# Kernel tuning notes

Hardware: AMD Instinct MI355X
Metric: run time of the kernel (lower is better)

The kernel has to match this reference:

```python
import jax, jax.numpy as jnp
import numpy as np

V, B, T, C, H, L = 32000, 4, 1024, 1024, 16, 8
HS = C // H  # head_size = 64


def _ln(x, g, b):
    m = x.mean(-1, keepdims=True)
    v = x.var(-1, keepdims=True)
    return (x - m) / jnp.sqrt(v + 1e-5) * g + b


def setup_inputs() -> dict:
    key = jax.random.key(0)
    ks = jax.random.split(key, 24)
    s = 0.02
    inp = {
        "idx": jax.random.randint(ks[0], (B, T), 0, V, dtype=jnp.int64),
        "tok_emb": jax.random.normal(ks[1], (V, C), jnp.float32) * s,
        "pos_emb": jax.random.normal(ks[2], (T, C), jnp.float32) * s,
        "Wq": jax.random.normal(ks[3], (L, H, C, HS), jnp.float32) * s,
        "Wk": jax.random.normal(ks[4], (L, H, C, HS), jnp.float32) * s,
        "Wv": jax.random.normal(ks[5], (L, H, C, HS), jnp.float32) * s,
        "Ph_w": jax.random.normal(ks[6], (L, H, HS, C), jnp.float32) * s,
        "Ph_b": jnp.zeros((L, H, C), jnp.float32),
        "Pm_w": jax.random.normal(ks[7], (L, C, C), jnp.float32) * s,
        "Pm_b": jnp.zeros((L, C), jnp.float32),
        "ln1_g": jnp.ones((L, C), jnp.float32),
        "ln1_b": jnp.zeros((L, C), jnp.float32),
        "ln2_g": jnp.ones((L, C), jnp.float32),
        "ln2_b": jnp.zeros((L, C), jnp.float32),
        "W1": jax.random.normal(ks[8], (L, C, 4 * C), jnp.float32) * s,
        "b1": jnp.zeros((L, 4 * C), jnp.float32),
        "W2": jax.random.normal(ks[9], (L, 4 * C, C), jnp.float32) * s,
        "b2": jnp.zeros((L, C), jnp.float32),
        "lnf_g": jnp.ones((C,), jnp.float32),
        "lnf_b": jnp.zeros((C,), jnp.float32),
        "head_w": jax.random.normal(ks[10], (C, V), jnp.float32) * s,
        "head_b": jnp.zeros((V,), jnp.float32),
    }
    return inp


def reference(idx, tok_emb, pos_emb, Wq, Wk, Wv, Ph_w, Ph_b, Pm_w, Pm_b,
              ln1_g, ln1_b, ln2_g, ln2_b, W1, b1, W2, b2, lnf_g, lnf_b,
              head_w, head_b):
    Bx, Tx = idx.shape
    x = tok_emb[idx] + pos_emb[:Tx]  # [B,T,C]
    mask = jnp.tril(jnp.ones((Tx, Tx), bool))
    scale = x.shape[-1] ** -0.5  # NOTE: original scales by n_embd**-0.5, not head_size
    n_layers = Wq.shape[0]
    for l in range(n_layers):
        xn = _ln(x, ln1_g[l], ln1_b[l])
        q = jnp.einsum('btc,hcs->bhts', xn, Wq[l])
        k = jnp.einsum('btc,hcs->bhts', xn, Wk[l])
        v = jnp.einsum('btc,hcs->bhts', xn, Wv[l])
        wei = jnp.einsum('bhts,bhus->bhtu', q, k) * scale
        wei = jnp.where(mask, wei, -jnp.inf)
        wei = jax.nn.softmax(wei, axis=-1)
        o = jnp.einsum('bhtu,bhus->bhts', wei, v)  # [B,H,T,HS]
        per = jnp.einsum('bhts,hsc->bhtc', o, Ph_w[l]) + Ph_b[l][None, :, None, :]
        sa = per.sum(axis=1) @ Pm_w[l] + Pm_b[l]  # combine heads, final proj
        x = x + sa
        xn2 = _ln(x, ln2_g[l], ln2_b[l])
        h = jax.nn.gelu(xn2 @ W1[l] + b1[l], approximate=False)
        x = x + h @ W2[l] + b2[l]
    x = _ln(x, lnf_g, lnf_b)
    return x @ head_w + head_b  # logits [B,T,V]
```

## Files before the change

kernel.cpp:

```cpp
#include <hip/hip_runtime.h>
#include <hip/hip_bf16.h>
#include <math.h>

static constexpr int V = 32000, B = 4, T = 1024, C = 1024, H = 16, NL = 8, HS = 64;
static constexpr int M = B * T;

typedef __bf16 bf16x8 __attribute__((ext_vector_type(8)));
typedef __bf16 bf16x4 __attribute__((ext_vector_type(4)));
typedef float f32x4 __attribute__((ext_vector_type(4)));

#define AS1 __attribute__((address_space(1)))
#define AS3 __attribute__((address_space(3)))

__global__ void k_embed(const int* __restrict__ idx, const float* __restrict__ tok,
                        const float* __restrict__ pos, float* __restrict__ x) {
  int g = blockIdx.x * blockDim.x + threadIdx.x;
  if (g >= M * C / 4) return;
  int c4 = g & 255;
  int bt = g >> 8;
  int t = bt & (T - 1);
  int row = idx[bt];
  float4 tv = *(const float4*)(tok + (size_t)row * C + c4 * 4);
  float4 pv = *(const float4*)(pos + (size_t)t * C + c4 * 4);
  float4 o;
  o.x = tv.x + pv.x; o.y = tv.y + pv.y; o.z = tv.z + pv.z; o.w = tv.w + pv.w;
  *(float4*)(x + (size_t)bt * C + c4 * 4) = o;
}

__global__ __launch_bounds__(256) void k_ln_bf(const float* __restrict__ x, const float* __restrict__ g,
                                               const float* __restrict__ b, __hip_bfloat16* __restrict__ y) {
  int row = blockIdx.x, tid = threadIdx.x;
  float4 v = ((const float4*)(x + (size_t)row * C))[tid];
  float s = v.x + v.y + v.z + v.w;
  float ss = v.x * v.x + v.y * v.y + v.z * v.z + v.w * v.w;
  for (int off = 32; off > 0; off >>= 1) {
    s += __shfl_down(s, off);
    ss += __shfl_down(ss, off);
  }
  __shared__ float sb[4], qb[4];
  int wid = tid >> 6;
  if ((tid & 63) == 0) { sb[wid] = s; qb[wid] = ss; }
  __syncthreads();
  float st = sb[0] + sb[1] + sb[2] + sb[3];
  float qt = qb[0] + qb[1] + qb[2] + qb[3];
  float mean = st * (1.0f / C);
  float var = qt * (1.0f / C) - mean * mean;
  float rstd = rsqrtf(var + 1e-5f);
  float4 gv = ((const float4*)g)[tid];
  float4 bv = ((const float4*)b)[tid];
  union { __hip_bfloat16 h[4]; ushort4 u; } pk;
  pk.h[0] = __float2bfloat16((v.x - mean) * rstd * gv.x + bv.x);
  pk.h[1] = __float2bfloat16((v.y - mean) * rstd * gv.y + bv.y);
  pk.h[2] = __float2bfloat16((v.z - mean) * rstd * gv.z + bv.z);
  pk.h[3] = __float2bfloat16((v.w - mean) * rstd * gv.w + bv.w);
  *(ushort4*)(y + (size_t)row * C + tid * 4) = pk.u;
}

__device__ __forceinline__ void transp_block(const float* __restrict__ in, __hip_bfloat16* __restrict__ out,
                                             int K, int N, int bx, int by, float (*t)[65]) {
  int n0 = bx * 64, k0 = by * 64;
  int tx = threadIdx.x & 15, ty = threadIdx.x >> 4;
#pragma unroll
  for (int i = 0; i < 64; i += 16) {
    float4 v = *(const float4*)(in + (size_t)(k0 + ty + i) * N + n0 + tx * 4);
    t[ty + i][tx * 4 + 0] = v.x;
    t[ty + i][tx * 4 + 1] = v.y;
    t[ty + i][tx * 4 + 2] = v.z;
    t[ty + i][tx * 4 + 3] = v.w;
  }
  __syncthreads();
#pragma unroll
  for (int i = 0; i < 64; i += 16) {
    int n = ty + i;
    union { __hip_bfloat16 h[4]; ushort4 u; } pk;
#pragma unroll
    for (int j = 0; j < 4; ++j) pk.h[j] = __float2bfloat16(t[tx * 4 + j][n]);
    *(ushort4*)(out + (size_t)(n0 + n) * K + k0 + tx * 4) = pk.u;
  }
}

__global__ __launch_bounds__(256) void k_transp(const float* __restrict__ in, __hip_bfloat16* __restrict__ out,
                                                int K, int N) {
  __shared__ float t[64][65];
  transp_block(in, out, K, N, blockIdx.x, blockIdx.y, t);
}

__global__ __launch_bounds__(256) void k_prep(const float* __restrict__ Wq, const float* __restrict__ Wk,
                                              const float* __restrict__ Wv, const float* __restrict__ Pm,
                                              const float* __restrict__ Ph, const float* __restrict__ W1,
                                              const float* __restrict__ W2,
                                              __hip_bfloat16* __restrict__ qkvw, __hip_bfloat16* __restrict__ pmT,
                                              __hip_bfloat16* __restrict__ phB, __hip_bfloat16* __restrict__ w1T,
                                              __hip_bfloat16* __restrict__ w2T) {
  __shared__ float tls[64][65];
  int bid = blockIdx.x;
  if (bid < 768) {
    int bx = bid & 15, z = bid >> 4;
    int sel = z >> 4, h = z & 15;
    const float* W = sel == 0 ? Wq : (sel == 1 ? Wk : Wv);
    const float* in = W + (size_t)h * C * HS;
    __hip_bfloat16* o = qkvw + ((size_t)sel * 1024 + h * 64) * C;
    int k0 = bx * 64;
    int tx = threadIdx.x & 15, ty = threadIdx.x >> 4;
#pragma unroll
    for (int i = 0; i < 64; i += 16) {
      float4 v = *(const float4*)(in + (size_t)(k0 + ty + i) * HS + tx * 4);
      tls[ty + i][tx * 4 + 0] = v.x;
      tls[ty + i][tx * 4 + 1] = v.y;
      tls[ty + i][tx * 4 + 2] = v.z;
      tls[ty + i][tx * 4 + 3] = v.w;
    }
    __syncthreads();
#pragma unroll
    for (int i = 0; i < 64; i += 16) {
      int n = ty + i;
      union { __hip_bfloat16 h4[4]; ushort4 u; } pk;
#pragma unroll
      for (int j = 0; j < 4; ++j) pk.h4[j] = __float2bfloat16(tls[tx * 4 + j][n]);
      *(ushort4*)(o + (size_t)n * C + k0 + tx * 4) = pk.u;
    }
  } else if (bid < 1024) {
    int r = bid - 768;
    transp_block(Pm, pmT, C, C, r & 15, r >> 4, tls);
  } else if (bid < 2048) {
    int g = (bid - 1024) * 256 + threadIdx.x;
    float4 v = ((const float4*)Ph)[g];
    union { __hip_bfloat16 h[4]; ushort4 u; } pk;
    pk.h[0] = __float2bfloat16(v.x);
    pk.h[1] = __float2bfloat16(v.y);
    pk.h[2] = __float2bfloat16(v.z);
    pk.h[3] = __float2bfloat16(v.w);
    ((ushort4*)phB)[g] = pk.u;
  } else if (bid < 3072) {
    int r = bid - 2048;
    transp_block(W1, w1T, C, 4 * C, r & 63, r >> 6, tls);
  } else {
    int r = bid - 3072;
    transp_block(W2, w2T, 4 * C, C, r & 15, r >> 4, tls);
  }
}

__global__ __launch_bounds__(256) void k_biasc(const float* __restrict__ phb, const float* __restrict__ Pm,
                                               const float* __restrict__ Pmb, float* __restrict__ bc) {
  __shared__ float bs[1024];
  __shared__ float red[4][64];
  int tid = threadIdx.x;
#pragma unroll
  for (int q = 0; q < 4; ++q) {
    int c = tid * 4 + q;
    float s = 0.0f;
    for (int h = 0; h < H; ++h) s += phb[(size_t)h * C + c];
    bs[c] = s;
  }
  __syncthreads();
  int c = blockIdx.x * 64 + (tid & 63);
  int part = tid >> 6;
  float s = 0.0f;
  for (int j = part * 256; j < part * 256 + 256; ++j) s += bs[j] * Pm[(size_t)j * C + c];
  red[part][tid & 63] = s;
  __syncthreads();
  if (tid < 64)
    bc[blockIdx.x * 64 + tid] = Pmb[blockIdx.x * 64 + tid] + red[0][tid] + red[1][tid] + red[2][tid] + red[3][tid];
}

template <int BIAS, int GELU, int RES, int OUTBF>
__global__ __launch_bounds__(256) void k_gemm_bf(const __hip_bfloat16* __restrict__ A,
                                                 const __hip_bfloat16* __restrict__ Bt,
                                                 void* Cout, const float* __restrict__ bias,
                                                 const float* res, int N, int K) {
  __shared__ __align__(16) __hip_bfloat16 As[128 * 32];
  __shared__ __align__(16) __hip_bfloat16 Bs[128 * 32];
  int bm = blockIdx.y * 128, bn = blockIdx.x * 128;
  int tid = threadIdx.x;
  int w = tid >> 6, l = tid & 63;
  int wr = (w >> 1) * 64, wc = (w & 1) * 64;
  int lr = l >> 2;
  int lk = (l & 3) * 8;
  int fr = l & 15;
  int fk = (l >> 4) * 8;
  const __hip_bfloat16* Ag = A + (size_t)bm * K;
  const __hip_bfloat16* Bg = Bt + (size_t)bn * K;
  f32x4 acc[4][4];
#pragma unroll
  for (int m = 0; m < 4; ++m)
#pragma unroll
    for (int n = 0; n < 4; ++n) acc[m][n] = (f32x4){0.f, 0.f, 0.f, 0.f};

  for (int k0 = 0; k0 < K; k0 += 32) {
    __syncthreads();
#pragma unroll
    for (int i = 0; i < 2; ++i) {
      int seg = w * 2 + i;
      int r = seg * 16 + lr;
      __builtin_amdgcn_global_load_lds((const AS1 void*)(Ag + (size_t)r * K + k0 + lk),
                                       (AS3 void*)(As + seg * 512), 16, 0, 0);
      __builtin_amdgcn_global_load_lds((const AS1 void*)(Bg + (size_t)r * K + k0 + lk),
                                       (AS3 void*)(Bs + seg * 512), 16, 0, 0);
    }
    __syncthreads();
    bf16x8 af[4], bfr[4];
#pragma unroll
    for (int m = 0; m < 4; ++m) af[m] = *(const bf16x8*)(As + ((size_t)(wr + m * 16 + fr)) * 32 + fk);
#pragma unroll
    for (int n = 0; n < 4; ++n) bfr[n] = *(const bf16x8*)(Bs + ((size_t)(wc + n * 16 + fr)) * 32 + fk);
#pragma unroll
    for (int m = 0; m < 4; ++m)
#pragma unroll
      for (int n = 0; n < 4; ++n)
        acc[m][n] = __builtin_amdgcn_mfma_f32_16x16x32_bf16(af[m], bfr[n], acc[m][n], 0, 0, 0);
  }
  int crow0 = (l >> 4) * 4;
  int ccol = l & 15;
#pragma unroll
  for (int m = 0; m < 4; ++m) {
    int row = bm + wr + m * 16 + crow0;
#pragma unroll
    for (int n = 0; n < 4; ++n) {
      int col = bn + wc + n * 16 + ccol;
      float bv = BIAS ? bias[col] : 0.0f;
#pragma unroll
      for (int r = 0; r < 4; ++r) {
        float v = acc[m][n][r] + bv;
        if (GELU) v = 0.5f * v * (1.0f + erff(v * 0.70710678118f));
        if (RES) v += res[(size_t)(row + r) * N + col];
        if (OUTBF)
          ((__hip_bfloat16*)Cout)[(size_t)(row + r) * N + col] = __float2bfloat16(v);
        else
          ((float*)Cout)[(size_t)(row + r) * N + col] = v;
      }
    }
  }
}

template <int BIAS, int GELU, int RES, int OUTBF>
__global__ __launch_bounds__(512, 2) void k_gemm256(const __hip_bfloat16* __restrict__ Ah,
                                                    const __hip_bfloat16* __restrict__ Bth,
                                                    void* Cout, const float* __restrict__ bias,
                                                    const float* res, int N, int K) {
  __shared__ __align__(16) __bf16 As[2][2 * 8192];
  __shared__ __align__(16) __bf16 Bs[2][2 * 8192];
  const __bf16* A = (const __bf16*)Ah;
  const __bf16* Bt = (const __bf16*)Bth;
  const int nx = N >> 8;
  const int bid = blockIdx.x;
  const int sw = ((bid & 7) * ((int)gridDim.x >> 3)) + (bid >> 3);
  const int bn = (sw % nx) << 8;
  const int bm = (sw / nx) << 8;
  const int tid = threadIdx.x, w = tid >> 6, l = tid & 63;
  const int wm = w >> 2, wn = w & 3;
  const int fr = l & 15, fg = l >> 4;
  const int srow = w * 32 + (l >> 2);
  const int scole = ((((l & 3) << 4) ^ ((l & 8) << 2) ^ (l & 16)) >> 1);
  const __bf16* Ag = A + (size_t)(bm + srow) * K + scole;
  const __bf16* Bg = Bt + (size_t)(bn + srow) * K + scole;
  const int arow = wm * 128 + fr;
  const int brow = wn * 64 + fr;
  const int kswz = ((fr & 2) << 4) | ((fr & 4) << 2);

  f32x4 acc[8][4];
#pragma unroll
  for (int m = 0; m < 8; ++m)
#pragma unroll
    for (int n = 0; n < 4; ++n) acc[m][n] = (f32x4){0.f, 0.f, 0.f, 0.f};

  auto stage = [&](int bufi, int half, int t) {
    size_t kb = (size_t)t * 64 + half * 32;
#pragma unroll
    for (int jj = 0; jj < 2; ++jj) {
      __builtin_amdgcn_global_load_lds((const AS1 void*)(Ag + (size_t)jj * 16 * K + kb),
                                       (AS3 void*)(&As[bufi][half * 8192 + (w * 32 + jj * 16) * 32]), 16, 0, 0);
      __builtin_amdgcn_global_load_lds((const AS1 void*)(Bg + (size_t)jj * 16 * K + kb),
                                       (AS3 void*)(&Bs[bufi][half * 8192 + (w * 32 + jj * 16) * 32]), 16, 0, 0);
    }
  };

#define RD_A(MG, HALF) \
  (*(const bf16x8*)(&As[cb][(HALF) * 8192 + (arow + (MG) * 16) * 32 + (((fg * 16) ^ kswz) >> 1)]))
#define RD_B(NG, HALF) \
  (*(const bf16x8*)(&Bs[cb][(HALF) * 8192 + (brow + (NG) * 16) * 32 + (((fg * 16) ^ kswz) >> 1)]))

  const int NT = K >> 6;
  stage(0, 0, 0);
  stage(0, 1, 0);

  for (int t = 0; t < NT; ++t) {
    const int cb = t & 1;
    const int nb = cb ^ 1;
    bf16x8 af[8], bv[4];

    asm volatile("s_waitcnt vmcnt(4)" ::: "memory");
    __builtin_amdgcn_s_barrier();
    __builtin_amdgcn_sched_barrier(0);
#pragma unroll
    for (int m = 0; m < 8; ++m) af[m] = RD_A(m, 0);
#pragma unroll
    for (int n = 0; n < 4; ++n) bv[n] = RD_B(n, 0);
    if (t + 1 < NT) stage(nb, 0, t + 1);
    __builtin_amdgcn_s_setprio(1);
#pragma unroll
    for (int m = 0; m < 8; ++m)
#pragma unroll
      for (int n = 0; n < 4; ++n)
        acc[m][n] = __builtin_amdgcn_mfma_f32_16x16x32_bf16(af[m], bv[n], acc[m][n], 0, 0, 0);
    __builtin_amdgcn_s_setprio(0);

    if (t + 1 < NT)
      asm volatile("s_waitcnt vmcnt(4)" ::: "memory");
    else
      asm volatile("s_waitcnt vmcnt(0)" ::: "memory");
    __builtin_amdgcn_s_barrier();
    __builtin_amdgcn_sched_barrier(0);
#pragma unroll
    for (int m = 0; m < 8; ++m) af[m] = RD_A(m, 1);
#pragma unroll
    for (int n = 0; n < 4; ++n) bv[n] = RD_B(n, 1);
    if (t + 1 < NT) stage(nb, 1, t + 1);
    __builtin_amdgcn_s_setprio(1);
#pragma unroll
    for (int m = 0; m < 8; ++m)
#pragma unroll
      for (int n = 0; n < 4; ++n)
        acc[m][n] = __builtin_amdgcn_mfma_f32_16x16x32_bf16(af[m], bv[n], acc[m][n], 0, 0, 0);
    __builtin_amdgcn_s_setprio(0);
  }
#undef RD_A
#undef RD_B

#pragma unroll
  for (int mg = 0; mg < 8; ++mg) {
    int row = bm + wm * 128 + mg * 16 + fg * 4;
#pragma unroll
    for (int n = 0; n < 4; ++n) {
      int col = bn + wn * 64 + n * 16 + fr;
      float bvx = BIAS ? bias[col] : 0.0f;
#pragma unroll
      for (int r = 0; r < 4; ++r) {
        float v = acc[mg][n][r] + bvx;
        if (GELU) v = 0.5f * v * (1.0f + erff(v * 0.70710678118f));
        if (RES) v += res[(size_t)(row + r) * N + col];
        if (OUTBF)
          ((__hip_bfloat16*)Cout)[(size_t)(row + r) * N + col] = __float2bfloat16(v);
        else
          ((float*)Cout)[(size_t)(row + r) * N + col] = v;
      }
    }
  }
}

__global__ __launch_bounds__(256) void k_attn(const __hip_bfloat16* __restrict__ qkvh,
                                              __hip_bfloat16* __restrict__ o) {
  const __bf16* qkv = (const __bf16*)qkvh;
  int qi = blockIdx.x;
  int bh = blockIdx.y;
  int b = bh >> 4, h = bh & 15;
  int tid = threadIdx.x;
  int w = tid >> 6, l = tid & 63;
  int fr = l & 15, fg = l >> 4;
  int qw = qi * 64 + w * 16;

  __shared__ __align__(16) __bf16 Ks[32][72];
  __shared__ __align__(16) __bf16 Vs[32][76];
  __shared__ __align__(16) __bf16 Ps[4][16][40];

  const size_t bT = (size_t)b * T;
  bf16x8 a_q[2];
  {
    const __bf16* qp = qkv + (bT + qw + fr) * 3072 + h * 64 + fg * 8;
    a_q[0] = *(const bf16x8*)qp;
    a_q[1] = *(const bf16x8*)(qp + 32);
  }
  f32x4 acc_o[4];
#pragma unroll
  for (int n = 0; n < 4; ++n) acc_o[n] = (f32x4){0.f, 0.f, 0.f, 0.f};
  float mrow[4] = {-1e30f, -1e30f, -1e30f, -1e30f};
  float lrow[4] = {0.f, 0.f, 0.f, 0.f};

  int sr = tid >> 3;
  int sc = (tid & 7) * 8;
  int ntile = (qi + 1) * 2;
  for (int t = 0; t < ntile; ++t) {
    int kv0 = t * 32;
    __syncthreads();
    {
      const __bf16* kp = qkv + (bT + kv0 + sr) * 3072 + 1024 + h * 64 + sc;
      bf16x8 k8 = *(const bf16x8*)kp;
      bf16x8 v8 = *(const bf16x8*)(kp + 1024);
      *(bf16x8*)&Ks[sr][sc] = k8;
      *(bf16x4*)&Vs[sr][sc] = __builtin_shufflevector(v8, v8, 0, 1, 2, 3);
      *(bf16x4*)&Vs[sr][sc + 4] = __builtin_shufflevector(v8, v8, 4, 5, 6, 7);
    }
    __syncthreads();
    if (kv0 > qw + 15) continue;

    f32x4 s0 = (f32x4){0.f, 0.f, 0.f, 0.f}, s1 = s0;
    s0 = __builtin_amdgcn_mfma_f32_16x16x32_bf16(a_q[0], *(const bf16x8*)&Ks[fr][fg * 8], s0, 0, 0, 0);
    s0 = __builtin_amdgcn_mfma_f32_16x16x32_bf16(a_q[1], *(const bf16x8*)&Ks[fr][32 + fg * 8], s0, 0, 0, 0);
    s1 = __builtin_amdgcn_mfma_f32_16x16x32_bf16(a_q[0], *(const bf16x8*)&Ks[16 + fr][fg * 8], s1, 0, 0, 0);
    s1 = __builtin_amdgcn_mfma_f32_16x16x32_bf16(a_q[1], *(const bf16x8*)&Ks[16 + fr][32 + fg * 8], s1, 0, 0, 0);

    int qrow = qw + fg * 4;
#pragma unroll
    for (int r = 0; r < 4; ++r) { s0[r] *= 0.03125f; s1[r] *= 0.03125f; }
    if (kv0 + 31 > qw) {
#pragma unroll
      for (int r = 0; r < 4; ++r) {
        if (kv0 + fr > qrow + r) s0[r] = -1e30f;
        if (kv0 + 16 + fr > qrow + r) s1[r] = -1e30f;
      }
    }
    float tm[4], psum[4], alpha[4];
#pragma unroll
    for (int r = 0; r < 4; ++r) tm[r] = fmaxf(s0[r], s1[r]);
#pragma unroll
    for (int off = 1; off < 16; off <<= 1)
#pragma unroll
      for (int r = 0; r < 4; ++r) tm[r] = fmaxf(tm[r], __shfl_xor(tm[r], off));
#pragma unroll
    for (int r = 0; r < 4; ++r) {
      float mnew = fmaxf(mrow[r], tm[r]);
      alpha[r] = __expf(mrow[r] - mnew);
      mrow[r] = mnew;
      float p0 = __expf(s0[r] - mnew);
      float p1 = __expf(s1[r] - mnew);
      s0[r] = p0; s1[r] = p1;
      psum[r] = p0 + p1;
    }
#pragma unroll
    for (int off = 1; off < 16; off <<= 1)
#pragma unroll
      for (int r = 0; r < 4; ++r) psum[r] += __shfl_xor(psum[r], off);
#pragma unroll
    for (int r = 0; r < 4; ++r) lrow[r] = lrow[r] * alpha[r] + psum[r];
#pragma unroll
    for (int n = 0; n < 4; ++n)
#pragma unroll
      for (int r = 0; r < 4; ++r) acc_o[n][r] *= alpha[r];

#pragma unroll
    for (int r = 0; r < 4; ++r) {
      Ps[w][fg * 4 + r][fr] = (__bf16)s0[r];
      Ps[w][fg * 4 + r][16 + fr] = (__bf16)s1[r];
    }
    bf16x8 a_p = *(const bf16x8*)&Ps[w][fr][fg * 8];
#pragma unroll
    for (int n = 0; n < 4; ++n) {
      bf16x8 bvv;
#pragma unroll
      for (int j = 0; j < 8; ++j) bvv[j] = Vs[fg * 8 + j][n * 16 + fr];
      acc_o[n] = __builtin_amdgcn_mfma_f32_16x16x32_bf16(a_p, bvv, acc_o[n], 0, 0, 0);
    }
  }
  float inv[4];
#pragma unroll
  for (int r = 0; r < 4; ++r) inv[r] = 1.0f / lrow[r];
  __bf16* ob = (__bf16*)o;
#pragma unroll
  for (int n = 0; n < 4; ++n)
#pragma unroll
    for (int r = 0; r < 4; ++r)
      ob[(bT + qw + fg * 4 + r) * 1024 + h * 64 + n * 16 + fr] = (__bf16)(acc_o[n][r] * inv[r]);
}

extern "C" void kernel_launch(void* const* d_in, const int* in_sizes, int n_in,
                              void* d_out, int out_size, void* d_ws, size_t ws_size,
                              hipStream_t stream) {
  const int* idx = (const int*)d_in[0];
  const float* tok = (const float*)d_in[1];
  const float* pos = (const float*)d_in[2];
  const float* Wq = (const float*)d_in[3];
  const float* Wk = (const float*)d_in[4];
  const float* Wv = (const float*)d_in[5];
  const float* Phw = (const float*)d_in[6];
  const float* Phb = (const float*)d_in[7];
  const float* Pmw = (const float*)d_in[8];
  const float* Pmb = (const float*)d_in[9];
  const float* ln1g = (const float*)d_in[10];
  const float* ln1b = (const float*)d_in[11];
  const float* ln2g = (const float*)d_in[12];
  const float* ln2b = (const float*)d_in[13];
  const float* W1 = (const float*)d_in[14];
  const float* b1 = (const float*)d_in[15];
  const float* W2 = (const float*)d_in[16];
  const float* b2 = (const float*)d_in[17];
  const float* lnfg = (const float*)d_in[18];
  const float* lnfb = (const float*)d_in[19];
  const float* headw = (const float*)d_in[20];
  const float* headb = (const float*)d_in[21];
  float* out = (float*)d_out;

  char* p = (char*)d_ws;
  float* x = (float*)p;                        p += (size_t)M * C * 4;
  float* bcv = (float*)p;                      p += 4096;
  char* layer_region = p;
  __hip_bfloat16* qkvb = (__hip_bfloat16*)p;   p += (size_t)M * 3072 * 2;
  __hip_bfloat16* ob = (__hip_bfloat16*)p;     p += (size_t)M * C * 2;
  __hip_bfloat16* hb = (__hip_bfloat16*)p;     p += (size_t)M * 4 * C * 2;
  __hip_bfloat16* xn = (__hip_bfloat16*)p;     p += (size_t)M * C * 2;
  __hip_bfloat16* qkvw = (__hip_bfloat16*)p;   p += (size_t)3 * C * C * 2;
  __hip_bfloat16* pmT = (__hip_bfloat16*)p;    p += (size_t)C * C * 2;
  __hip_bfloat16* phB = (__hip_bfloat16*)p;    p += (size_t)C * C * 2;
  __hip_bfloat16* wcombT = (__hip_bfloat16*)p; p += (size_t)C * C * 2;
  __hip_bfloat16* w1T = (__hip_bfloat16*)p;    p += (size_t)4 * C * C * 2;
  __hip_bfloat16* w2T = (__hip_bfloat16*)p;    p += (size_t)4 * C * C * 2;
  __hip_bfloat16* wt_head = (__hip_bfloat16*)layer_region;

  k_embed<<<(M * C / 4 + 255) / 256, 256, 0, stream>>>(idx, tok, pos, x);

  for (int l = 0; l < NL; ++l) {
    k_ln_bf<<<M, 256, 0, stream>>>(x, ln1g + (size_t)l * C, ln1b + (size_t)l * C, xn);
    k_prep<<<4096, 256, 0, stream>>>(Wq + (size_t)l * H * C * HS, Wk + (size_t)l * H * C * HS,
                                     Wv + (size_t)l * H * C * HS, Pmw + (size_t)l * C * C,
                                     Phw + (size_t)l * H * HS * C, W1 + (size_t)l * C * 4 * C,
                                     W2 + (size_t)l * 4 * C * C, qkvw, pmT, phB, w1T, w2T);
    k_gemm256<0, 0, 0, 1><<<(3072 / 256) * (M / 256), 512, 0, stream>>>(xn, qkvw, qkvb, nullptr, nullptr, 3072, C);
    k_attn<<<dim3(T / 64, B * H), 256, 0, stream>>>(qkvb, ob);
    k_biasc<<<16, 256, 0, stream>>>(Phb + (size_t)l * H * C, Pmw + (size_t)l * C * C, Pmb + (size_t)l * C, bcv);
    k_gemm_bf<0, 0, 0, 1><<<dim3(C / 128, C / 128), 256, 0, stream>>>(pmT, phB, wcombT, nullptr, nullptr, C, C);
    k_gemm_bf<1, 0, 1, 0><<<dim3(C / 128, M / 128), 256, 0, stream>>>(ob, wcombT, x, bcv, x, C, C);
    k_ln_bf<<<M, 256, 0, stream>>>(x, ln2g + (size_t)l * C, ln2b + (size_t)l * C, xn);
    k_gemm256<1, 1, 0, 1><<<(4 * C / 256) * (M / 256), 512, 0, stream>>>(xn, w1T, hb, b1 + (size_t)l * 4 * C, nullptr, 4 * C, C);
    k_gemm_bf<1, 0, 1, 0><<<dim3(C / 128, M / 128), 256, 0, stream>>>(hb, w2T, x, b2 + (size_t)l * C, x, C, 4 * C);
  }

  k_ln_bf<<<M, 256, 0, stream>>>(x, lnfg, lnfb, xn);
  k_transp<<<dim3(500, 16), 256, 0, stream>>>(headw, wt_head, C, V);
  k_gemm256<1, 0, 0, 0><<<(V / 256) * (M / 256), 512, 0, stream>>>(xn, wt_head, out, headb, nullptr, V, C);
}
```

Before: 3.588 ms.

## Use triple-buffered K=32 LDS pipeline with prefetch distance two in 256 GEMM

The 256x256 GEMM changes from two buffers of K=64 (each split into two halves) to three rotating LDS buffers of K=32, issuing loads two k-steps ahead. This keeps one barrier per K=32 step but gives global loads more time to land before they are consumed, and LDS use drops from 128KB to 96KB. The trade-off is twice as many loop iterations and barriers per K extent, with fewer MFMAs between each sync.

```diff
diff --git a/kernel.cpp b/kernel.cpp
--- a/kernel.cpp
+++ b/kernel.cpp
@@ -237,8 +237,8 @@
                                                     const __hip_bfloat16* __restrict__ Bth,
                                                     void* Cout, const float* __restrict__ bias,
                                                     const float* res, int N, int K) {
-  __shared__ __align__(16) __bf16 As[2][2 * 8192];
-  __shared__ __align__(16) __bf16 Bs[2][2 * 8192];
+  __shared__ __align__(16) __bf16 As[3][256 * 32];
+  __shared__ __align__(16) __bf16 Bs[3][256 * 32];
   const __bf16* A = (const __bf16*)Ah;
   const __bf16* Bt = (const __bf16*)Bth;
   const int nx = N >> 8;
@@ -255,7 +255,7 @@
   const __bf16* Bg = Bt + (size_t)(bn + srow) * K + scole;
   const int arow = wm * 128 + fr;
   const int brow = wn * 64 + fr;
-  const int kswz = ((fr & 2) << 4) | ((fr & 4) << 2);
+  const int koff = (((fg * 16) ^ (((fr & 2) << 4) | ((fr & 4) << 2))) >> 1);
 
   f32x4 acc[8][4];
 #pragma unroll
@@ -263,68 +263,50 @@
 #pragma unroll
     for (int n = 0; n < 4; ++n) acc[m][n] = (f32x4){0.f, 0.f, 0.f, 0.f};
 
-  auto stage = [&](int bufi, int half, int t) {
-    size_t kb = (size_t)t * 64 + half * 32;
+  auto stage = [&](int bufi, int tt) {
+    size_t kb = (size_t)tt * 32;
 #pragma unroll
     for (int jj = 0; jj < 2; ++jj) {
       __builtin_amdgcn_global_load_lds((const AS1 void*)(Ag + (size_t)jj * 16 * K + kb),
-                                       (AS3 void*)(&As[bufi][half * 8192 + (w * 32 + jj * 16) * 32]), 16, 0, 0);
+                                       (AS3 void*)(&As[bufi][(w * 32 + jj * 16) * 32]), 16, 0, 0);
       __builtin_amdgcn_global_load_lds((const AS1 void*)(Bg + (size_t)jj * 16 * K + kb),
-                                       (AS3 void*)(&Bs[bufi][half * 8192 + (w * 32 + jj * 16) * 32]), 16, 0, 0);
+                                       (AS3 void*)(&Bs[bufi][(w * 32 + jj * 16) * 32]), 16, 0, 0);
     }
   };
 
-#define RD_A(MG, HALF) \
-  (*(const bf16x8*)(&As[cb][(HALF) * 8192 + (arow + (MG) * 16) * 32 + (((fg * 16) ^ kswz) >> 1)]))
-#define RD_B(NG, HALF) \
-  (*(const bf16x8*)(&Bs[cb][(HALF) * 8192 + (brow + (NG) * 16) * 32 + (((fg * 16) ^ kswz) >> 1)]))
-
-  const int NT = K >> 6;
-  stage(0, 0, 0);
-  stage(0, 1, 0);
-
+  const int NT = K >> 5;
+  stage(0, 0);
+  stage(1, 1);
+  asm volatile("s_waitcnt vmcnt(4)" ::: "memory");
+  __builtin_amdgcn_sched_barrier(0);
+  __builtin_amdgcn_s_barrier();
+  __builtin_amdgcn_sched_barrier(0);
+
+  int cb = 0;
   for (int t = 0; t < NT; ++t) {
-    const int cb = t & 1;
-    const int nb = cb ^ 1;
-    bf16x8 af[8], bv[4];
-
-    asm volatile("s_waitcnt vmcnt(4)" ::: "memory");
-    __builtin_amdgcn_s_barrier();
-    __builtin_amdgcn_sched_barrier(0);
-#pragma unroll
-    for (int m = 0; m < 8; ++m) af[m] = RD_A(m, 0);
-#pragma unroll
-    for (int n = 0; n < 4; ++n) bv[n] = RD_B(n, 0);
-    if (t + 1 < NT) stage(nb, 0, t + 1);
+    int pb = cb + 2 >= 3 ? cb - 1 : cb + 2;
+    if (t + 2 < NT) stage(pb, t + 2);
+    bf16x8 fa[8], fb[4];
+#pragma unroll
+    for (int mg = 0; mg < 8; ++mg) fa[mg] = *(const bf16x8*)(&As[cb][(arow + mg * 16) * 32 + koff]);
+#pragma unroll
+    for (int ng = 0; ng < 4; ++ng) fb[ng] = *(const bf16x8*)(&Bs[cb][(brow + ng * 16) * 32 + koff]);
     __builtin_amdgcn_s_setprio(1);
 #pragma unroll
-    for (int m = 0; m < 8; ++m)
-#pragma unroll
-      for (int n = 0; n < 4; ++n)
-        acc[m][n] = __builtin_amdgcn_mfma_f32_16x16x32_bf16(af[m], bv[n], acc[m][n], 0, 0, 0);
+    for (int mg = 0; mg < 8; ++mg)
+#pragma unroll
+      for (int ng = 0; ng < 4; ++ng)
+        acc[mg][ng] = __builtin_amdgcn_mfma_f32_16x16x32_bf16(fa[mg], fb[ng], acc[mg][ng], 0, 0, 0);
     __builtin_amdgcn_s_setprio(0);
-
-    if (t + 1 < NT)
+    if (t + 2 < NT)
       asm volatile("s_waitcnt vmcnt(4)" ::: "memory");
     else
       asm volatile("s_waitcnt vmcnt(0)" ::: "memory");
+    __builtin_amdgcn_sched_barrier(0);
     __builtin_amdgcn_s_barrier();
     __builtin_amdgcn_sched_barrier(0);
-#pragma unroll
-    for (int m = 0; m < 8; ++m) af[m] = RD_A(m, 1);
-#pragma unroll
-    for (int n = 0; n < 4; ++n) bv[n] = RD_B(n, 1);
-    if (t + 1 < NT) stage(nb, 1, t + 1);
-    __builtin_amdgcn_s_setprio(1);
-#pragma unroll
-    for (int m = 0; m < 8; ++m)
-#pragma unroll
-      for (int n = 0; n < 4; ++n)
-        acc[m][n] = __builtin_amdgcn_mfma_f32_16x16x32_bf16(af[m], bv[n], acc[m][n], 0, 0, 0);
-    __builtin_amdgcn_s_setprio(0);
-  }
-#undef RD_A
-#undef RD_B
+    cb = cb + 1 >= 3 ? 0 : cb + 1;
+  }
 
 #pragma unroll
   for (int mg = 0; mg < 8; ++mg) {
```

Result: slower. 3.837 ms (+6.9%).
